# Kernel optimization log

Hardware: AMD Instinct MI355X
Metric: run time of the kernel (lower is better)

Reference implementation:

```python
import jax, jax.numpy as jnp
import numpy as np

B, N, C, K1, K2, TD = 4, 4096, 128, 16, 8, 64
CIN = 2 * (3 + C)  # 262


def setup_inputs() -> dict:
    key = jax.random.key(0)
    ks = jax.random.split(key, 8)
    s = 0.05
    feature = jax.random.normal(ks[0], (B, C, N), jnp.float32)
    xyz = jax.random.normal(ks[1], (B, 3, N), jnp.float32)
    wq = jax.random.normal(ks[2], (TD, CIN), jnp.float32) * s
    wk = jax.random.normal(ks[3], (TD, CIN), jnp.float32) * s
    wv = jax.random.normal(ks[4], (TD, CIN), jnp.float32) * s
    w1 = jax.random.normal(ks[5], (C, TD), jnp.float32) * s
    bq = jnp.zeros((TD,), jnp.float32)
    bk = jnp.zeros((TD,), jnp.float32)
    bv = jnp.zeros((TD,), jnp.float32)
    b1 = jnp.zeros((C,), jnp.float32)
    return {"feature": feature, "xyz": xyz, "wq": wq, "bq": bq,
            "wk": wk, "bk": bk, "wv": wv, "bv": bv, "w1": w1, "b1": b1}


def _group(x, ind):
    # x: [B, Cx, N], ind: [B, N, K] -> [B, Cx, K, N]; g[b,c,k,n] = x[b,c,ind[b,n,k]]
    g = jnp.take_along_axis(x[:, :, None, :], ind[:, None, :, :], axis=3)  # [B,Cx,N,K]
    return g.transpose(0, 1, 3, 2)


def reference(feature, xyz, wq, bq, wk, bk, wv, bv, w1, b1):
    # --- KNN (self-included then dropped), idx[b,n,k] = k-th nearest of point n ---
    sq = jnp.sum(xyz * xyz, axis=1)                                   # [B,N]
    dist = sq[:, :, None] + sq[:, None, :] - 2.0 * jnp.einsum('bdn,bdm->bnm', xyz, xyz)
    _, idx = jax.lax.top_k(-dist, K1 + 1)                             # [B,N,17]
    idx = idx[:, :, 1:]                                               # drop self -> [B,N,16]
    idx1 = idx[:, :, :K2]                                             # [B,N,8]

    gxyz = _group(xyz, idx)        # [B,3,16,N]
    gxyz1 = _group(xyz, idx1)      # [B,3,8,N]
    gfea = _group(feature, idx)    # [B,C,16,N]
    gfea1 = _group(feature, idx1)  # [B,C,8,N]

    rel_xyz = gxyz - xyz[:, :, None, :]
    rel_xyz1 = gxyz1 - xyz[:, :, None, :]
    rel_fea = gfea - feature[:, :, None, :]
    rel_fea1 = gfea1 - feature[:, :, None, :]

    def relpos(rx, rf, K):
        return jnp.concatenate([
            rx,
            jnp.broadcast_to(xyz[:, :, None, :], (B, 3, K, N)),
            rf,
            jnp.broadcast_to(feature[:, :, None, :], (B, C, K, N)),
        ], axis=1)  # [B,262,K,N]

    rel_pos = relpos(rel_xyz, rel_fea, K1)     # [B,262,16,N]
    rel_pos1 = relpos(rel_xyz1, rel_fea1, K2)  # [B,262,8,N]

    # 1x1 Conv2d projections
    q = jnp.einsum('oc,bckn->bokn', wq, rel_pos1) + bq[None, :, None, None]  # [B,64,8,N]
    k = jnp.einsum('oc,bckn->bokn', wk, rel_pos) + bk[None, :, None, None]   # [B,64,16,N]
    v = jnp.einsum('oc,bckn->bokn', wv, rel_pos) + bv[None, :, None, None]   # [B,64,16,N]

    attn = jnp.einsum('bmnf,bmjf->bnjf', q, k)   # [B,8,16,N]
    attn = jax.nn.softmax(attn, axis=-2)         # softmax over j (16 neighbors)
    res = jnp.einsum('bnjf,bmjf->bmf', attn, v)  # [B,64,N]

    out = jnp.einsum('om,bmf->bof', w1, res) + b1[None, :, None]  # Conv1d 64->128
    return out + feature
```

## Files before the change

kernel.cpp:

```cpp
#include <hip/hip_runtime.h>

#define NN 4096
#define CCH 128

typedef float f2 __attribute__((ext_vector_type(2)));

__global__ __launch_bounds__(256) void transpose_w(
    const float* __restrict__ wq, const float* __restrict__ wk, const float* __restrict__ wv,
    const float* __restrict__ w1, const float* __restrict__ xyz,
    float* __restrict__ wTq, float* __restrict__ wTk, float* __restrict__ wTv,
    float* __restrict__ w1T, float* __restrict__ wPack, float4* __restrict__ pts4,
    float* __restrict__ pp) {
  int t = blockIdx.x * 256 + threadIdx.x;
  if (t < 64 * 262) {
    int o = t / 262, c = t - o * 262;
    wTq[c * 64 + o] = wq[t];
    wTk[c * 64 + o] = wk[t];
    wTv[c * 64 + o] = wv[t];
  }
  if (t < 128 * 64) {
    int r = t >> 6, c2 = t & 63;
    w1T[c2 * 128 + r] = w1[t];
  }
  if (t < 49152) {
    int c  = t & 3;
    int o  = (t >> 2) & 63;
    int ph = (t >> 8) & 1;
    int t2 = t >> 9;
    int mm = t2 % 3;
    int t3 = t2 / 3;
    int ct = t3 & 15;
    int half = t3 >> 4;
    const float* wsrc = (mm == 0) ? wq : ((mm == 1) ? wk : wv);
    int isT = c & 1;
    int rr  = 2 * ph + (c >> 1);
    int col = (isT ? 134 : 6) + 4 * (half * 16 + ct) + rr;
    wPack[t] = wsrc[o * 262 + col];
  }
  if (t < 4 * NN) {
    int bb = t >> 12, i = t & 4095;
    const float* xb = xyz + (size_t)bb * 3 * NN;
    float x = xb[i], y = xb[NN + i], z = xb[2 * NN + i];
    float w = x * x + y * y + z * z;
    pts4[t] = make_float4(x, y, z, w);
    float* pb = pp + ((size_t)bb * 2048 + (i >> 1)) * 8 + (i & 1);
    pb[0] = x; pb[2] = y; pb[4] = z; pb[6] = w;
  }
}

__global__ __launch_bounds__(1024, 4) void knn_half(const float4* __restrict__ pts4,
                                                    const float* __restrict__ pp,
                                                    unsigned long long* __restrict__ keys_ws) {
  __shared__ float bufA[64 * 64];
  __shared__ float bufB[64 * 64];
  __shared__ unsigned long long hits[32 * 65];
  __shared__ int cnt[64];
  const int b  = blockIdx.x >> 7;
  const int g  = (blockIdx.x >> 1) & 63;
  const int h  = blockIdx.x & 1;
  const int n0 = g << 6;
  const int ql = threadIdx.x & 63;
  const int ch = __builtin_amdgcn_readfirstlane(threadIdx.x >> 6);
  if (threadIdx.x < 64) cnt[threadIdx.x] = 0;
  const int q = n0 + ql;
  const float4* pb4 = pts4 + ((size_t)b << 12);
  const float4 me = pb4[q];
  const f2 mex = {me.x, me.x}, mey = {me.y, me.y}, mez = {me.z, me.z}, mew = {me.w, me.w};
  const f2 mneg2 = {-2.0f, -2.0f};
  const float* ppb = pp + ((size_t)b << 14);
  const int m0 = (h << 11) + (ch << 7);
  const bool ovl = (((h << 4) + ch) == (n0 >> 7));
  float bd0 = 3.0e38f, bd1 = 3.0e38f, bd2 = 3.0e38f, bd3 = 3.0e38f;
  for (int mb = m0; mb < m0 + 128; mb += 8) {
    const f2* pg2 = reinterpret_cast<const f2*>(ppb + (size_t)mb * 4);
    f2 d2[4];
#pragma unroll
    for (int u = 0; u < 4; ++u) {
      f2 X = pg2[u * 4 + 0], Y = pg2[u * 4 + 1], Z = pg2[u * 4 + 2], W = pg2[u * 4 + 3];
      f2 dot = X * mex + Y * mey + Z * mez;
      d2[u] = dot * mneg2 + (W + mew);
    }
    if (ovl) {
#pragma unroll
      for (int u = 0; u < 4; ++u) {
        d2[u].x = (mb + 2 * u     == q) ? 3.0e38f : d2[u].x;
        d2[u].y = (mb + 2 * u + 1 == q) ? 3.0e38f : d2[u].y;
      }
    }
#pragma unroll
    for (int u = 0; u < 4; ++u) {
#pragma unroll
      for (int e = 0; e < 2; ++e) {
        float d = e ? d2[u].y : d2[u].x;
        bd3 = __builtin_amdgcn_fmed3f(d, bd2, bd3);
        bd2 = __builtin_amdgcn_fmed3f(d, bd1, bd2);
        bd1 = __builtin_amdgcn_fmed3f(d, bd0, bd1);
        bd0 = fminf(bd0, d);
      }
    }
  }
  {
    const int r0 = (ch * 4) * 64 + ql;
    bufA[r0] = bd0; bufA[r0 + 64] = bd1; bufA[r0 + 128] = bd2; bufA[r0 + 192] = bd3;
  }
  __syncthreads();
  if (ch < 8) {
    const int a0 = (2 * ch) * 4, b0 = (2 * ch + 1) * 4;
    float o8[8]; int pa = 0, pb = 0;
#pragma unroll
    for (int k = 0; k < 8; ++k) {
      float va = (pa < 4) ? bufA[(a0 + pa) * 64 + ql] : 3.0e38f;
      float vb = (pb < 4) ? bufA[(b0 + pb) * 64 + ql] : 3.0e38f;
      bool ta = va <= vb;
      o8[k] = ta ? va : vb;
      pa += ta ? 1 : 0; pb += ta ? 0 : 1;
    }
#pragma unroll
    for (int k = 0; k < 8; ++k) bufB[(ch * 8 + k) * 64 + ql] = o8[k];
  }
  __syncthreads();
  if (ch < 4) {
    const int a0 = (2 * ch) * 8, b0 = (2 * ch + 1) * 8;
    float o16[16]; int pa = 0, pb = 0;
#pragma unroll
    for (int k = 0; k < 16; ++k) {
      float va = (pa < 8) ? bufB[(a0 + pa) * 64 + ql] : 3.0e38f;
      float vb = (pb < 8) ? bufB[(b0 + pb) * 64 + ql] : 3.0e38f;
      bool ta = va <= vb;
      o16[k] = ta ? va : vb;
      pa += ta ? 1 : 0; pb += ta ? 0 : 1;
    }
#pragma unroll
    for (int k = 0; k < 16; ++k) bufA[(ch * 16 + k) * 64 + ql] = o16[k];
  }
  __syncthreads();
  if (ch < 2) {
    const int a0 = (2 * ch) * 16, b0 = (2 * ch + 1) * 16;
    float o16[16]; int pa = 0, pb = 0;
#pragma unroll
    for (int k = 0; k < 16; ++k) {
      float va = bufA[(a0 + pa) * 64 + ql];
      float vb = bufA[(b0 + pb) * 64 + ql];
      bool ta = va <= vb;
      o16[k] = ta ? va : vb;
      pa += ta ? 1 : 0; pb += ta ? 0 : 1;
    }
#pragma unroll
    for (int k = 0; k < 16; ++k) bufB[(ch * 16 + k) * 64 + ql] = o16[k];
  }
  __syncthreads();
  if (ch == 0) {
    float v = 0.f; int pa = 0, pb = 0;
#pragma unroll
    for (int k = 0; k < 16; ++k) {
      float va = bufB[pa * 64 + ql];
      float vb = bufB[(16 + pb) * 64 + ql];
      bool ta = va <= vb;
      v = ta ? va : vb;
      pa += ta ? 1 : 0; pb += ta ? 0 : 1;
    }
    bufA[15 * 64 + ql] = v;
  }
  __syncthreads();
  const float tau = bufA[15 * 64 + ql];
  for (int mb = m0; mb < m0 + 128; mb += 8) {
    const f2* pg2 = reinterpret_cast<const f2*>(ppb + (size_t)mb * 4);
#pragma unroll
    for (int u = 0; u < 4; ++u) {
      f2 X = pg2[u * 4 + 0], Y = pg2[u * 4 + 1], Z = pg2[u * 4 + 2], W = pg2[u * 4 + 3];
      f2 dot = X * mex + Y * mey + Z * mez;
      f2 d2 = dot * mneg2 + (W + mew);
      if (fminf(d2.x, d2.y) <= tau) {
        if (d2.x <= tau && (mb + 2 * u) != q) {
          int pos = atomicAdd(&cnt[ql], 1);
          if (pos < 32) {
            unsigned int f = __float_as_uint(d2.x);
            f ^= (f >> 31) ? 0xFFFFFFFFu : 0x80000000u;
            hits[pos * 65 + ql] = ((unsigned long long)f << 32) | (unsigned int)(mb + 2 * u);
          }
        }
        if (d2.y <= tau && (mb + 2 * u + 1) != q) {
          int pos = atomicAdd(&cnt[ql], 1);
          if (pos < 32) {
            unsigned int f = __float_as_uint(d2.y);
            f ^= (f >> 31) ? 0xFFFFFFFFu : 0x80000000u;
            hits[pos * 65 + ql] = ((unsigned long long)f << 32) | (unsigned int)(mb + 2 * u + 1);
          }
        }
      }
    }
  }
  __syncthreads();
  const int l5 = threadIdx.x & 31;
#pragma unroll
  for (int t = 0; t < 2; ++t) {
    const int qq = (t * 1024 + (int)threadIdx.x) >> 5;
    int nv = cnt[qq]; nv = nv > 32 ? 32 : nv;
    unsigned long long key = (l5 < nv) ? hits[l5 * 65 + qq] : ~0ULL;
#pragma unroll
    for (int k = 2; k <= 32; k <<= 1) {
#pragma unroll
      for (int jm = k >> 1; jm > 0; jm >>= 1) {
        unsigned long long o2 = __shfl_xor(key, jm, 32);
        bool asc = ((l5 & k) == 0);
        bool lower = ((l5 & jm) == 0);
        unsigned long long mn = key < o2 ? key : o2;
        unsigned long long mx = key < o2 ? o2 : key;
        key = (lower == asc) ? mn : mx;
      }
    }
    if (l5 < 16) {
      const size_t gq = (size_t)((b << 12) + n0 + qq);
      keys_ws[((size_t)h << 18) + gq * 16 + l5] = key;
    }
  }
}

__global__ __launch_bounds__(512) void proj_kernel(
    const float* __restrict__ feature, const float* __restrict__ xyz,
    const float* __restrict__ wTq, const float* __restrict__ wTk, const float* __restrict__ wTv,
    const float* __restrict__ wPack,
    const float* __restrict__ bq, const float* __restrict__ bk, const float* __restrict__ bv,
    float* __restrict__ uqA, float* __restrict__ cq,
    float2* __restrict__ ukv,
    float* __restrict__ ck, float* __restrict__ cv) {
  __shared__ float fl[64][132];
  __shared__ float4 wl[16 * 3 * 2 * 64];
  const int p0 = blockIdx.x << 6;
  const int b  = p0 >> 12;
  const int n0 = p0 & 4095;
  {
    const int i  = threadIdx.x & 63;
    const int c0 = threadIdx.x >> 6;
    const float* fb = feature + (size_t)b * CCH * NN + n0 + i;
    for (int cc = c0; cc < CCH; cc += 8) fl[i][cc] = fb[(size_t)cc * NN];
    if (threadIdx.x < 192) {
      const int d = threadIdx.x >> 6;
      fl[i][128 + d] = xyz[((size_t)b * 3 + d) * NN + n0 + i];
    }
  }
  const int o  = threadIdx.x & 63;
  const int pg = threadIdx.x >> 6;
  const float4* wp = reinterpret_cast<const float4*>(wPack);
  f2 acc[3][8];
#pragma unroll
  for (int mm = 0; mm < 3; ++mm)
#pragma unroll
    for (int s = 0; s < 8; ++s) acc[mm][s] = (f2){0.f, 0.f};

  for (int half = 0; half < 2; ++half) {
    __syncthreads();
    for (int d4 = threadIdx.x; d4 < 6144; d4 += 512)
      wl[d4] = wp[half * 6144 + d4];
    __syncthreads();
#pragma unroll 4
    for (int ct = 0; ct < 16; ++ct) {
      float4 wA[3], wB[3];
#pragma unroll
      for (int mm = 0; mm < 3; ++mm) {
        wA[mm] = wl[((ct * 3 + mm) * 2 + 0) * 64 + o];
        wB[mm] = wl[((ct * 3 + mm) * 2 + 1) * 64 + o];
      }
      const int cglob = half * 16 + ct;
#pragma unroll
      for (int s = 0; s < 8; ++s) {
        const float4 f4 = *reinterpret_cast<const float4*>(&fl[pg * 8 + s][4 * cglob]);
        const f2 sx = {f4.x, f4.x}, sy = {f4.y, f4.y}, sz = {f4.z, f4.z}, sw = {f4.w, f4.w};
#pragma unroll
        for (int mm = 0; mm < 3; ++mm) {
          const f2* a2 = reinterpret_cast<const f2*>(&wA[mm]);
          const f2* b2 = reinterpret_cast<const f2*>(&wB[mm]);
          f2 a = acc[mm][s];
          a += sx * a2[0];
          a += sy * a2[1];
          a += sz * b2[0];
          a += sw * b2[1];
          acc[mm][s] = a;
        }
      }
    }
  }
  float wxu[3][3], wxt[3][3];
#pragma unroll
  for (int dd = 0; dd < 3; ++dd) {
    wxu[0][dd] = wTq[dd * 64 + o]; wxt[0][dd] = wTq[(3 + dd) * 64 + o];
    wxu[1][dd] = wTk[dd * 64 + o]; wxt[1][dd] = wTk[(3 + dd) * 64 + o];
    wxu[2][dd] = wTv[dd * 64 + o]; wxt[2][dd] = wTv[(3 + dd) * 64 + o];
  }
  const float bo0 = bq[o], bo1 = bk[o], bo2 = bv[o];
#pragma unroll
  for (int s = 0; s < 8; ++s) {
    const int p = pg * 8 + s;
    const float x = fl[p][128], y = fl[p][129], z = fl[p][130];
    const size_t gp = ((size_t)(p0 + p)) * 64 + o;
    float uu, tt;
    uu = acc[0][s].x + wxu[0][0] * x + wxu[0][1] * y + wxu[0][2] * z;
    tt = acc[0][s].y + wxt[0][0] * x + wxt[0][1] * y + wxt[0][2] * z;
    uqA[gp] = uu; cq[gp] = tt + bo0 - uu;
    const float uk_ = acc[1][s].x + wxu[1][0] * x + wxu[1][1] * y + wxu[1][2] * z;
    tt = acc[1][s].y + wxt[1][0] * x + wxt[1][1] * y + wxt[1][2] * z;
    ck[gp] = tt + bo1 - uk_;
    const float uv_ = acc[2][s].x + wxu[2][0] * x + wxu[2][1] * y + wxu[2][2] * z;
    tt = acc[2][s].y + wxt[2][0] * x + wxt[2][1] * y + wxt[2][2] * z;
    cv[gp] = tt + bo2 - uv_;
    ukv[gp] = make_float2(uk_, uv_);
  }
}

__global__ __launch_bounds__(256) void attn_core(
    const unsigned long long* __restrict__ keys_ws,
    const float* __restrict__ uqA, const float* __restrict__ cq,
    const float2* __restrict__ ukv,
    const float* __restrict__ ck, const float* __restrict__ cv,
    float* __restrict__ res_ws) {
  __shared__ float kq[4][24][68];
  const int slot = threadIdx.x >> 6;
  const int o    = threadIdx.x & 63;
  const int p = (blockIdx.x << 2) + slot;
  const int b = p >> 12;
  const int l5 = o & 31;
  unsigned long long key =
      (l5 < 16) ? keys_ws[(size_t)p * 16 + l5]
                : keys_ws[((size_t)1 << 18) + (size_t)p * 16 + (31 - l5)];
#pragma unroll
  for (int jm = 16; jm > 0; jm >>= 1) {
    unsigned long long o2 = __shfl_xor(key, jm, 32);
    bool lower = ((l5 & jm) == 0);
    unsigned long long mn = key < o2 ? key : o2;
    unsigned long long mx = key < o2 ? o2 : key;
    key = lower ? mn : mx;
  }
  const int kidx = (int)(key & 0xFFFFFFFFu);
  const size_t pb = (size_t)p * 64 + o;
  const float cqo = cq[pb], cko = ck[pb], cvo = cv[pb];
  const int rowbase = (b << 12) * 64;
  float v[16];
#pragma unroll
  for (int j = 0; j < 16; ++j) {
    int nb = __shfl(kidx, j);
    int row = rowbase + nb * 64 + o;
    float2 kv = ukv[row];
    kq[slot][j][o] = kv.x + cko;
    v[j] = kv.y + cvo;
    if (j < 8) kq[slot][16 + j][o] = uqA[row] + cqo;
  }
  const int i  = o >> 3;
  const int jj = o & 7;
  const float* qrow = &kq[slot][16 + i][0];
  const float* k0r  = &kq[slot][jj][0];
  const float* k1r  = &kq[slot][8 + jj][0];
  float s0 = 0.f, s1 = 0.f;
#pragma unroll
  for (int t = 0; t < 16; ++t) {
    float4 q4 = *reinterpret_cast<const float4*>(qrow + 4 * t);
    float4 a4 = *reinterpret_cast<const float4*>(k0r + 4 * t);
    float4 c4 = *reinterpret_cast<const float4*>(k1r + 4 * t);
    s0 += q4.x * a4.x + q4.y * a4.y + q4.z * a4.z + q4.w * a4.w;
    s1 += q4.x * c4.x + q4.y * c4.y + q4.z * c4.z + q4.w * c4.w;
  }
  float mx = fmaxf(s0, s1);
  mx = fmaxf(mx, __shfl_xor(mx, 1));
  mx = fmaxf(mx, __shfl_xor(mx, 2));
  mx = fmaxf(mx, __shfl_xor(mx, 4));
  float e0 = __expf(s0 - mx), e1 = __expf(s1 - mx);
  float den = e0 + e1;
  den += __shfl_xor(den, 1);
  den += __shfl_xor(den, 2);
  den += __shfl_xor(den, 4);
  const float inv = 1.0f / den;
  float w0 = e0 * inv, w1s = e1 * inv;
  w0 += __shfl_xor(w0, 8);   w1s += __shfl_xor(w1s, 8);
  w0 += __shfl_xor(w0, 16);  w1s += __shfl_xor(w1s, 16);
  w0 += __shfl_xor(w0, 32);  w1s += __shfl_xor(w1s, 32);
  float res = 0.f;
#pragma unroll
  for (int j = 0; j < 8; ++j) {
    res += __shfl(w0, j)  * v[j];
    res += __shfl(w1s, j) * v[j + 8];
  }
  res_ws[pb] = res;
}

__global__ __launch_bounds__(512) void out_kernel(
    const float* __restrict__ feature, const float* __restrict__ res,
    const float* __restrict__ w1T, const float* __restrict__ b1,
    float* __restrict__ out) {
  __shared__ float rT[64][66];
  const int p0 = blockIdx.x << 6;
  const int b  = p0 >> 12;
  const int n0 = p0 & 4095;
  {
    const int o = threadIdx.x & 63;
    for (int pp = threadIdx.x >> 6; pp < 64; pp += 8)
      rT[o][pp] = res[(size_t)(p0 + pp) * 64 + o];
  }
  __syncthreads();
  const int n = threadIdx.x & 63;
  const int c0 = (threadIdx.x >> 6) * 16;
  float acc[16];
#pragma unroll
  for (int cc = 0; cc < 16; ++cc) acc[cc] = b1[c0 + cc];
  for (int o = 0; o < 64; ++o) {
    const float rr = rT[o][n];
    const float* wrow = &w1T[o * 128 + c0];
#pragma unroll
    for (int cc = 0; cc < 16; ++cc) acc[cc] += wrow[cc] * rr;
  }
#pragma unroll
  for (int cc = 0; cc < 16; ++cc) {
    const size_t gi = ((size_t)(b * 128 + c0 + cc) << 12) + n0 + n;
    out[gi] = acc[cc] + feature[gi];
  }
}

extern "C" void kernel_launch(void* const* d_in, const int* in_sizes, int n_in,
                              void* d_out, int out_size, void* d_ws, size_t ws_size,
                              hipStream_t stream) {
  const float* feature = (const float*)d_in[0];
  const float* xyz     = (const float*)d_in[1];
  const float* wq      = (const float*)d_in[2];
  const float* bq      = (const float*)d_in[3];
  const float* wk      = (const float*)d_in[4];
  const float* bk      = (const float*)d_in[5];
  const float* wv      = (const float*)d_in[6];
  const float* bv      = (const float*)d_in[7];
  const float* w1      = (const float*)d_in[8];
  const float* b1      = (const float*)d_in[9];
  float* out = (float*)d_out;

  char* ws = (char*)d_ws;
  float4* pts4 = (float4*)(ws + (1u << 20));
  float*  pp   = (float*)(ws + (1u << 20) + 262144);
  float*  uqA  = (float*)(ws + (2u << 20));
  float*  cq   = (float*)(ws + (6u << 20));
  float*  ck   = (float*)(ws + (10u << 20));
  float*  cv   = (float*)(ws + (14u << 20));
  float2* ukv  = (float2*)(ws + (18u << 20));
  float*  res  = (float*)(ws + (26u << 20));
  float*  wTq  = (float*)(ws + (30u << 20));
  float*  wTk  = wTq + 262 * 64;
  float*  wTv  = wTk + 262 * 64;
  float*  w1T  = wTv + 262 * 64;
  float*  wPk  = w1T + 128 * 64;
  unsigned long long* keys = (unsigned long long*)(ws + (31u << 20));

  transpose_w<<<192, 256, 0, stream>>>(wq, wk, wv, w1, xyz, wTq, wTk, wTv, w1T, wPk, pts4, pp);
  knn_half<<<512, 1024, 0, stream>>>(pts4, pp, keys);
  proj_kernel<<<256, 512, 0, stream>>>(feature, xyz, wTq, wTk, wTv, wPk, bq, bk, bv,
                                       uqA, cq, ukv, ck, cv);
  attn_core<<<4096, 256, 0, stream>>>(keys, uqA, cq, ukv, ck, cv, res);
  out_kernel<<<256, 512, 0, stream>>>(feature, res, w1T, b1, out);
}
```

Measured before the change: 198.8 us.

## Split KNN top-4 tracking into four independent chains and use bitonic merges

```diff
diff --git a/kernel.cpp b/kernel.cpp
--- a/kernel.cpp
+++ b/kernel.cpp
@@ -4,6 +4,29 @@
 #define CCH 128
 
 typedef float f2 __attribute__((ext_vector_type(2)));
+typedef float f4 __attribute__((ext_vector_type(4)));
+
+__device__ __forceinline__ void cmpex(float& x, float& y) {
+  float mn = fminf(x, y);
+  y = fmaxf(x, y);
+  x = mn;
+}
+
+template <int N>
+__device__ __forceinline__ void bitonic_merge(float* s) {
+#pragma unroll
+  for (int jm = N / 2; jm > 0; jm >>= 1)
+#pragma unroll
+    for (int i = 0; i < N; ++i)
+      if ((i & jm) == 0) cmpex(s[i], s[i + jm]);
+}
+
+__device__ __forceinline__ void merge44(float* a, const float* b) {
+  float m0 = fminf(a[0], b[3]), m1 = fminf(a[1], b[2]);
+  float m2 = fminf(a[2], b[1]), m3 = fminf(a[3], b[0]);
+  cmpex(m0, m2); cmpex(m1, m3); cmpex(m0, m1); cmpex(m2, m3);
+  a[0] = m0; a[1] = m1; a[2] = m2; a[3] = m3;
+}
 
 __global__ __launch_bounds__(256) void transpose_w(
     const float* __restrict__ wq, const float* __restrict__ wk, const float* __restrict__ wv,
@@ -70,13 +93,17 @@
   const float* ppb = pp + ((size_t)b << 14);
   const int m0 = (h << 11) + (ch << 7);
   const bool ovl = (((h << 4) + ch) == (n0 >> 7));
-  float bd0 = 3.0e38f, bd1 = 3.0e38f, bd2 = 3.0e38f, bd3 = 3.0e38f;
+  float t0[4], t1[4], t2[4], t3[4];
+#pragma unroll
+  for (int u = 0; u < 4; ++u) { t0[u] = 3.0e38f; t1[u] = 3.0e38f; t2[u] = 3.0e38f; t3[u] = 3.0e38f; }
+#pragma unroll 2
   for (int mb = m0; mb < m0 + 128; mb += 8) {
-    const f2* pg2 = reinterpret_cast<const f2*>(ppb + (size_t)mb * 4);
+    const f4* pg4 = reinterpret_cast<const f4*>(ppb + (size_t)mb * 4);
     f2 d2[4];
 #pragma unroll
     for (int u = 0; u < 4; ++u) {
-      f2 X = pg2[u * 4 + 0], Y = pg2[u * 4 + 1], Z = pg2[u * 4 + 2], W = pg2[u * 4 + 3];
+      f4 A = pg4[2 * u], B = pg4[2 * u + 1];
+      f2 X = A.xy, Y = A.zw, Z = B.xy, W = B.zw;
       f2 dot = X * mex + Y * mey + Z * mez;
       d2[u] = dot * mneg2 + (W + mew);
     }
@@ -89,85 +116,78 @@
     }
 #pragma unroll
     for (int u = 0; u < 4; ++u) {
-#pragma unroll
-      for (int e = 0; e < 2; ++e) {
-        float d = e ? d2[u].y : d2[u].x;
-        bd3 = __builtin_amdgcn_fmed3f(d, bd2, bd3);
-        bd2 = __builtin_amdgcn_fmed3f(d, bd1, bd2);
-        bd1 = __builtin_amdgcn_fmed3f(d, bd0, bd1);
-        bd0 = fminf(bd0, d);
-      }
-    }
-  }
+      float* bd = (u == 0) ? t0 : (u == 1) ? t1 : (u == 2) ? t2 : t3;
+      float dx = d2[u].x, dy = d2[u].y;
+      bd[3] = __builtin_amdgcn_fmed3f(dx, bd[2], bd[3]);
+      bd[2] = __builtin_amdgcn_fmed3f(dx, bd[1], bd[2]);
+      bd[1] = __builtin_amdgcn_fmed3f(dx, bd[0], bd[1]);
+      bd[0] = fminf(bd[0], dx);
+      bd[3] = __builtin_amdgcn_fmed3f(dy, bd[2], bd[3]);
+      bd[2] = __builtin_amdgcn_fmed3f(dy, bd[1], bd[2]);
+      bd[1] = __builtin_amdgcn_fmed3f(dy, bd[0], bd[1]);
+      bd[0] = fminf(bd[0], dy);
+    }
+  }
+  merge44(t0, t1); merge44(t2, t3); merge44(t0, t2);
   {
     const int r0 = (ch * 4) * 64 + ql;
-    bufA[r0] = bd0; bufA[r0 + 64] = bd1; bufA[r0 + 128] = bd2; bufA[r0 + 192] = bd3;
+    bufA[r0] = t0[0]; bufA[r0 + 64] = t0[1]; bufA[r0 + 128] = t0[2]; bufA[r0 + 192] = t0[3];
   }
   __syncthreads();
   if (ch < 8) {
-    const int a0 = (2 * ch) * 4, b0 = (2 * ch + 1) * 4;
-    float o8[8]; int pa = 0, pb = 0;
-#pragma unroll
-    for (int k = 0; k < 8; ++k) {
-      float va = (pa < 4) ? bufA[(a0 + pa) * 64 + ql] : 3.0e38f;
-      float vb = (pb < 4) ? bufA[(b0 + pb) * 64 + ql] : 3.0e38f;
-      bool ta = va <= vb;
-      o8[k] = ta ? va : vb;
-      pa += ta ? 1 : 0; pb += ta ? 0 : 1;
-    }
-#pragma unroll
-    for (int k = 0; k < 8; ++k) bufB[(ch * 8 + k) * 64 + ql] = o8[k];
+    const int base = 8 * ch;
+    float s[8];
+#pragma unroll
+    for (int i = 0; i < 4; ++i) s[i] = bufA[(base + i) * 64 + ql];
+#pragma unroll
+    for (int i = 0; i < 4; ++i) s[4 + i] = bufA[(base + 7 - i) * 64 + ql];
+    bitonic_merge<8>(s);
+#pragma unroll
+    for (int i = 0; i < 8; ++i) bufB[(base + i) * 64 + ql] = s[i];
   }
   __syncthreads();
   if (ch < 4) {
-    const int a0 = (2 * ch) * 8, b0 = (2 * ch + 1) * 8;
-    float o16[16]; int pa = 0, pb = 0;
-#pragma unroll
-    for (int k = 0; k < 16; ++k) {
-      float va = (pa < 8) ? bufB[(a0 + pa) * 64 + ql] : 3.0e38f;
-      float vb = (pb < 8) ? bufB[(b0 + pb) * 64 + ql] : 3.0e38f;
-      bool ta = va <= vb;
-      o16[k] = ta ? va : vb;
-      pa += ta ? 1 : 0; pb += ta ? 0 : 1;
-    }
-#pragma unroll
-    for (int k = 0; k < 16; ++k) bufA[(ch * 16 + k) * 64 + ql] = o16[k];
+    const int base = 16 * ch;
+    float s[16];
+#pragma unroll
+    for (int i = 0; i < 8; ++i) s[i] = bufB[(base + i) * 64 + ql];
+#pragma unroll
+    for (int i = 0; i < 8; ++i) s[8 + i] = bufB[(base + 15 - i) * 64 + ql];
+    bitonic_merge<16>(s);
+#pragma unroll
+    for (int i = 0; i < 16; ++i) bufA[(base + i) * 64 + ql] = s[i];
   }
   __syncthreads();
   if (ch < 2) {
-    const int a0 = (2 * ch) * 16, b0 = (2 * ch + 1) * 16;
-    float o16[16]; int pa = 0, pb = 0;
-#pragma unroll
-    for (int k = 0; k < 16; ++k) {
-      float va = bufA[(a0 + pa) * 64 + ql];
-      float vb = bufA[(b0 + pb) * 64 + ql];
-      bool ta = va <= vb;
-      o16[k] = ta ? va : vb;
-      pa += ta ? 1 : 0; pb += ta ? 0 : 1;
-    }
-#pragma unroll
-    for (int k = 0; k < 16; ++k) bufB[(ch * 16 + k) * 64 + ql] = o16[k];
+    const int base = 32 * ch;
+    float l[16];
+#pragma unroll
+    for (int i = 0; i < 16; ++i)
+      l[i] = fminf(bufA[(base + i) * 64 + ql], bufA[(base + 31 - i) * 64 + ql]);
+    bitonic_merge<16>(l);
+#pragma unroll
+    for (int i = 0; i < 16; ++i) bufB[(16 * ch + i) * 64 + ql] = l[i];
   }
   __syncthreads();
   if (ch == 0) {
-    float v = 0.f; int pa = 0, pb = 0;
-#pragma unroll
-    for (int k = 0; k < 16; ++k) {
-      float va = bufB[pa * 64 + ql];
-      float vb = bufB[(16 + pb) * 64 + ql];
-      bool ta = va <= vb;
-      v = ta ? va : vb;
-      pa += ta ? 1 : 0; pb += ta ? 0 : 1;
-    }
-    bufA[15 * 64 + ql] = v;
+    float m[16];
+#pragma unroll
+    for (int i = 0; i < 16; ++i)
+      m[i] = fminf(bufB[i * 64 + ql], bufB[(31 - i) * 64 + ql]);
+    float t = m[0];
+#pragma unroll
+    for (int i = 1; i < 16; ++i) t = fmaxf(t, m[i]);
+    bufA[15 * 64 + ql] = t;
   }
   __syncthreads();
   const float tau = bufA[15 * 64 + ql];
+#pragma unroll 2
   for (int mb = m0; mb < m0 + 128; mb += 8) {
-    const f2* pg2 = reinterpret_cast<const f2*>(ppb + (size_t)mb * 4);
+    const f4* pg4 = reinterpret_cast<const f4*>(ppb + (size_t)mb * 4);
 #pragma unroll
     for (int u = 0; u < 4; ++u) {
-      f2 X = pg2[u * 4 + 0], Y = pg2[u * 4 + 1], Z = pg2[u * 4 + 2], W = pg2[u * 4 + 3];
+      f4 A = pg4[2 * u], B = pg4[2 * u + 1];
+      f2 X = A.xy, Y = A.zw, Z = B.xy, W = B.zw;
       f2 dot = X * mex + Y * mey + Z * mez;
       f2 d2 = dot * mneg2 + (W + mew);
       if (fminf(d2.x, d2.y) <= tau) {
@@ -264,8 +284,8 @@
       const int cglob = half * 16 + ct;
 #pragma unroll
       for (int s = 0; s < 8; ++s) {
-        const float4 f4 = *reinterpret_cast<const float4*>(&fl[pg * 8 + s][4 * cglob]);
-        const f2 sx = {f4.x, f4.x}, sy = {f4.y, f4.y}, sz = {f4.z, f4.z}, sw = {f4.w, f4.w};
+        const float4 f4w = *reinterpret_cast<const float4*>(&fl[pg * 8 + s][4 * cglob]);
+        const f2 sx = {f4w.x, f4w.x}, sy = {f4w.y, f4w.y}, sz = {f4w.z, f4w.z}, sw = {f4w.w, f4w.w};
 #pragma unroll
         for (int mm = 0; mm < 3; ++mm) {
           const f2* a2 = reinterpret_cast<const f2*>(&wA[mm]);
```

After: 196.7 us. Within noise of the previous version (-1.1%).
